# Kernel optimization log

Measured on AMD Instinct MI355X. Metric: run time of the kernel, lower is better.

The kernel has to match this reference:

```python
import jax, jax.numpy as jnp
import numpy as np

B, N, D_IN, D_OUT = 2, 4096, 768, 768


def setup_inputs() -> dict:
    key = jax.random.key(0)
    kx, kq, kk, kv = jax.random.split(key, 4)
    x = jax.random.normal(kx, (B, N, D_IN), dtype=jnp.float32)
    # Linear(d_in, d_out, bias=False) weights, stored as [d_in, d_out]
    scale = 1.0 / np.sqrt(D_IN)
    Wq = jax.random.normal(kq, (D_IN, D_OUT), dtype=jnp.float32) * scale
    Wk = jax.random.normal(kk, (D_IN, D_OUT), dtype=jnp.float32) * scale
    Wv = jax.random.normal(kv, (D_IN, D_OUT), dtype=jnp.float32) * scale
    return {"x": x, "Wq": Wq, "Wk": Wk, "Wv": Wv}


def reference(x, Wq, Wk, Wv):
    # q,k,v: [B, N, D_OUT]
    q = jnp.einsum('bnd,de->bne', x, Wq)
    k = jnp.einsum('bnd,de->bne', x, Wk)
    v = jnp.einsum('bnd,de->bne', x, Wv)
    # Full [B, N, N] score matrix (naive attention, as in source).
    # NOTE: source's masked_fill is non-in-place and discarded, so NO causal
    # mask is actually applied -- reproduced faithfully here.
    scores = jnp.einsum('bqe,bke->bqk', q, k) / jnp.sqrt(jnp.float32(k.shape[-1]))
    weights = jax.nn.softmax(scores, axis=-1)
    # dropout rate 0.0 / eval mode -> identity
    out = jnp.einsum('bqk,bke->bqe', weights, v)  # [B, N, D_OUT]
    return out
```

## Files before the change

kernel.cpp:

```cpp
#include <hip/hip_runtime.h>

typedef __bf16 bf16x8 __attribute__((ext_vector_type(8)));
typedef float f32x4 __attribute__((ext_vector_type(4)));
typedef unsigned short us8 __attribute__((ext_vector_type(8)));

#define GAS __attribute__((address_space(1)))
#define LAS __attribute__((address_space(3)))

__device__ __forceinline__ unsigned short f32_to_bf16(float f) {
    unsigned int u = __float_as_uint(f);
    u += 0x7FFFu + ((u >> 16) & 1u);
    return (unsigned short)(u >> 16);
}

__device__ __forceinline__ float bf16_to_f32(unsigned short h) {
    return __uint_as_float((unsigned int)h << 16);
}

__device__ __forceinline__ void load16(const unsigned short* g, unsigned short* l) {
    __builtin_amdgcn_global_load_lds((GAS unsigned int*)g, (LAS unsigned int*)l, 16, 0, 0);
}

__global__ __launch_bounds__(1024) void prep(
    const float* __restrict__ x, unsigned short* __restrict__ Xbf,
    const float* __restrict__ W0, const float* __restrict__ W1, const float* __restrict__ W2,
    unsigned short* __restrict__ T0, unsigned short* __restrict__ T1, unsigned short* __restrict__ T2)
{
    __shared__ float tile[32][33];
    const int id = blockIdx.x;
    const int t = threadIdx.x;
    if (id < 1536) {
        int i = id * 1024 + t;
        float4 v = ((const float4*)x)[i];
        ushort4 o;
        o.x = f32_to_bf16(v.x); o.y = f32_to_bf16(v.y);
        o.z = f32_to_bf16(v.z); o.w = f32_to_bf16(v.w);
        ((ushort4*)Xbf)[i] = o;
    } else {
        const int tid = id - 1536;
        const int z = tid / 576, rem = tid % 576;
        const int by = rem / 24, bx = rem % 24;
        const float* W = (z == 0) ? W0 : (z == 1) ? W1 : W2;
        unsigned short* T = (z == 0) ? T0 : (z == 1) ? T1 : T2;
        const int r0 = by * 32, c0 = bx * 32;
        const int tx = t & 31, ty = t >> 5;
        tile[ty][tx] = W[(size_t)(r0 + ty) * 768 + c0 + tx];
        __syncthreads();
        T[(size_t)(c0 + ty) * 768 + r0 + tx] = f32_to_bf16(tile[tx][ty]);
    }
}

__device__ __forceinline__ void qk_body(
    unsigned short* smem, int f,
    const unsigned short* __restrict__ Xbf, const unsigned short* __restrict__ Wqk,
    unsigned short* __restrict__ Qb, unsigned short* __restrict__ Kb)
{
    const int xcd = f & 7;
    const int local = f >> 3;
    const int mb = xcd * 4 + (local >> 3);
    const int nb = local & 7;
    unsigned short* AsP[2] = { smem, smem + 16384 };
    unsigned short* BsP[2] = { smem + 32768, smem + 32768 + 12288 };
    const unsigned short* A = Xbf;
    const unsigned short* B = Wqk;
    unsigned short* C = (nb < 4) ? Qb : Kb;
    const int m0 = mb * 256;
    const int n0 = nb * 192;
    const int c0 = (nb & 3) * 192;
    const int lda = 768, ldb = 768, ldc = 768;
    constexpr int NT = 12;

    const int t = threadIdx.x;
    const int lane = t & 63;
    const int w = t >> 6;
    const int wm = (w >> 2) * 128;
    const int wn = (w & 3) * 48;
    const int r15 = lane & 15;
    const int qa = lane >> 4;

    const unsigned short* srcA[4];
    int dstA[4];
#pragma unroll
    for (int i = 0; i < 4; ++i) {
        const int c = i * 512 + t;
        const int row = c >> 3;
        const int cc = (c & 7) ^ (row & 7);
        srcA[i] = A + (size_t)(m0 + row) * lda + cc * 8;
        dstA[i] = c * 8;
    }
    const unsigned short* srcB[3];
    int dstB[3];
#pragma unroll
    for (int i = 0; i < 3; ++i) {
        const int c = i * 512 + t;
        const int row = c >> 3;
        const int cc = (c & 7) ^ (row & 7);
        srcB[i] = B + (size_t)(n0 + row) * ldb + cc * 8;
        dstB[i] = c * 8;
    }

    auto stage = [&](int buf, int kbase) {
#pragma unroll
        for (int i = 0; i < 4; ++i) load16(srcA[i] + kbase, &AsP[buf][dstA[i]]);
#pragma unroll
        for (int i = 0; i < 3; ++i) load16(srcB[i] + kbase, &BsP[buf][dstB[i]]);
    };

    int offA[8][2], offB[3][2];
#pragma unroll
    for (int mi = 0; mi < 8; ++mi) {
        const int row = wm + mi * 16 + r15;
#pragma unroll
        for (int ks = 0; ks < 2; ++ks)
            offA[mi][ks] = row * 64 + (((ks << 2) + qa) ^ (row & 7)) * 8;
    }
#pragma unroll
    for (int ni = 0; ni < 3; ++ni) {
        const int row = wn + ni * 16 + r15;
#pragma unroll
        for (int ks = 0; ks < 2; ++ks)
            offB[ni][ks] = row * 64 + (((ks << 2) + qa) ^ (row & 7)) * 8;
    }

    f32x4 acc[8][3];
#pragma unroll
    for (int i = 0; i < 8; ++i)
#pragma unroll
        for (int j = 0; j < 3; ++j) acc[i][j] = (f32x4){0.f, 0.f, 0.f, 0.f};

    stage(0, 0);
    stage(1, 64);

    for (int tt = 0; tt < NT; ++tt) {
        const int b = tt & 1;
        if (tt == NT - 1) {
            asm volatile("s_waitcnt vmcnt(0)" ::: "memory");
        } else {
            asm volatile("s_waitcnt vmcnt(7)" ::: "memory");
        }
        __builtin_amdgcn_s_barrier();

#pragma unroll
        for (int ks = 0; ks < 2; ++ks) {
            bf16x8 aA[8], bB[3];
#pragma unroll
            for (int i = 0; i < 8; ++i)
                aA[i] = *(const bf16x8*)&AsP[b][offA[i][ks]];
#pragma unroll
            for (int ni = 0; ni < 3; ++ni)
                bB[ni] = *(const bf16x8*)&BsP[b][offB[ni][ks]];
#pragma unroll
            for (int i = 0; i < 8; ++i)
#pragma unroll
                for (int ni = 0; ni < 3; ++ni)
                    acc[i][ni] = __builtin_amdgcn_mfma_f32_16x16x32_bf16(
                        aA[i], bB[ni], acc[i][ni], 0, 0, 0);
        }

        asm volatile("" ::: "memory");
        __builtin_amdgcn_s_barrier();

        if (tt + 2 < NT) stage(b, (tt + 2) << 6);
    }

    const int cr = (lane >> 4) * 4;
#pragma unroll
    for (int mi = 0; mi < 8; ++mi)
#pragma unroll
        for (int ni = 0; ni < 3; ++ni) {
            const int gm = m0 + wm + mi * 16 + cr;
            const int gn = c0 + wn + ni * 16 + r15;
#pragma unroll
            for (int r = 0; r < 4; ++r)
                C[(size_t)(gm + r) * ldc + gn] = f32_to_bf16(acc[mi][ni][r]);
        }
}

__device__ __forceinline__ void vt_body(
    unsigned short* smem, int f,
    const unsigned short* __restrict__ WvT, const unsigned short* __restrict__ Xbf,
    unsigned short* __restrict__ Vt)
{
    const int xcd = f & 7;
    const int local = f >> 3;
    const int nb = xcd * 8 + (local >> 2);
    const int mb = local & 3;
    unsigned short* AsP[2] = { smem, smem + 12288 };
    unsigned short* BsP[2] = { smem + 24576, smem + 24576 + 8192 };
    const unsigned short* A = WvT;
    const unsigned short* B = Xbf;
    unsigned short* C = Vt;
    const int m0 = mb * 192;
    const int n0 = nb * 128;
    const int lda = 768, ldb = 768, ldc = 8192;
    constexpr int NT = 12;

    const int t = threadIdx.x;
    const int lane = t & 63;
    const int w = t >> 6;
    const int wm = (w >> 2) * 96;
    const int wn = (w & 3) * 32;
    const int r15 = lane & 15;
    const int qa = lane >> 4;

    const unsigned short* srcA[3];
    int dstA[3];
#pragma unroll
    for (int i = 0; i < 3; ++i) {
        const int c = i * 512 + t;
        const int row = c >> 3;
        const int cc = (c & 7) ^ (row & 7);
        srcA[i] = A + (size_t)(m0 + row) * lda + cc * 8;
        dstA[i] = c * 8;
    }
    const unsigned short* srcB[2];
    int dstB[2];
#pragma unroll
    for (int i = 0; i < 2; ++i) {
        const int c = i * 512 + t;
        const int row = c >> 3;
        const int cc = (c & 7) ^ (row & 7);
        srcB[i] = B + (size_t)(n0 + row) * ldb + cc * 8;
        dstB[i] = c * 8;
    }

    auto stage = [&](int buf, int kbase) {
#pragma unroll
        for (int i = 0; i < 3; ++i) load16(srcA[i] + kbase, &AsP[buf][dstA[i]]);
#pragma unroll
        for (int i = 0; i < 2; ++i) load16(srcB[i] + kbase, &BsP[buf][dstB[i]]);
    };

    int offA[6][2], offB[2][2];
#pragma unroll
    for (int mi = 0; mi < 6; ++mi) {
        const int row = wm + mi * 16 + r15;
#pragma unroll
        for (int ks = 0; ks < 2; ++ks)
            offA[mi][ks] = row * 64 + (((ks << 2) + qa) ^ (row & 7)) * 8;
    }
#pragma unroll
    for (int ni = 0; ni < 2; ++ni) {
        const int row = wn + ni * 16 + r15;
#pragma unroll
        for (int ks = 0; ks < 2; ++ks)
            offB[ni][ks] = row * 64 + (((ks << 2) + qa) ^ (row & 7)) * 8;
    }

    f32x4 acc[6][2];
#pragma unroll
    for (int i = 0; i < 6; ++i)
#pragma unroll
        for (int j = 0; j < 2; ++j) acc[i][j] = (f32x4){0.f, 0.f, 0.f, 0.f};

    stage(0, 0);
    stage(1, 64);

    for (int tt = 0; tt < NT; ++tt) {
        const int b = tt & 1;
        if (tt == NT - 1) {
            asm volatile("s_waitcnt vmcnt(0)" ::: "memory");
        } else {
            asm volatile("s_waitcnt vmcnt(5)" ::: "memory");
        }
        __builtin_amdgcn_s_barrier();

#pragma unroll
        for (int ks = 0; ks < 2; ++ks) {
            bf16x8 aA[6], bB[2];
#pragma unroll
            for (int i = 0; i < 6; ++i)
                aA[i] = *(const bf16x8*)&AsP[b][offA[i][ks]];
#pragma unroll
            for (int ni = 0; ni < 2; ++ni)
                bB[ni] = *(const bf16x8*)&BsP[b][offB[ni][ks]];
#pragma unroll
            for (int i = 0; i < 6; ++i)
#pragma unroll
                for (int ni = 0; ni < 2; ++ni)
                    acc[i][ni] = __builtin_amdgcn_mfma_f32_16x16x32_bf16(
                        aA[i], bB[ni], acc[i][ni], 0, 0, 0);
        }

        asm volatile("" ::: "memory");
        __builtin_amdgcn_s_barrier();

        if (tt + 2 < NT) stage(b, (tt + 2) << 6);
    }

    const int cr = (lane >> 4) * 4;
#pragma unroll
    for (int mi = 0; mi < 6; ++mi)
#pragma unroll
        for (int ni = 0; ni < 2; ++ni) {
            const int gm = m0 + wm + mi * 16 + cr;
            const int gn = n0 + wn + ni * 16 + r15;
#pragma unroll
            for (int r = 0; r < 4; ++r)
                C[(size_t)(gm + r) * ldc + gn] = f32_to_bf16(acc[mi][ni][r]);
        }
}

__global__ __launch_bounds__(512) void qkv3(
    const unsigned short* __restrict__ Xbf,
    const unsigned short* __restrict__ Wqk,
    unsigned short* __restrict__ Qb,
    unsigned short* __restrict__ Kb,
    unsigned short* __restrict__ Vt)
{
    __shared__ unsigned short smem[57344];
    const int f = blockIdx.x;
    if (f < 256) qk_body(smem, f, Xbf, Wqk, Qb, Kb);
    else         vt_body(smem, f - 256, Wqk + 1179648, Xbf, Vt);
}

__global__ __launch_bounds__(512) void gemm_s_exp2(
    const unsigned short* __restrict__ Q, const unsigned short* __restrict__ Kb,
    unsigned short* __restrict__ Sexp, float alpha)
{
    const int f = blockIdx.x;
    const int xcd = f & 7;
    const int local = f >> 3;
    const int x = (xcd & 1) * 8 + (local & 7);
    const int y = ((xcd >> 1) & 1) * 8 + (local >> 3);
    const int bb = xcd >> 2;
    const unsigned short* A = Q + (size_t)bb * 3145728;
    const unsigned short* B = Kb + (size_t)bb * 3145728;
    unsigned short* C = Sexp + (size_t)bb * 16777216;
    const int m0 = y * 256, n0 = x * 256;
    const int lda = 768, ldb = 768, ldc = 4096;
    constexpr int NT = 12;

    __shared__ unsigned short As[2][256 * 64];
    __shared__ unsigned short Bs[2][256 * 64];

    const int t = threadIdx.x;
    const int lane = t & 63;
    const int w = t >> 6;
    const int wm = (w >> 2) * 128;
    const int wn = (w & 3) * 64;
    const int r15 = lane & 15;
    const int qa = lane >> 4;

    const unsigned short* srcA[4];
    const unsigned short* srcB[4];
    int dst[4];
#pragma unroll
    for (int i = 0; i < 4; ++i) {
        const int c = i * 512 + t;
        const int row = c >> 3;
        const int cc = (c & 7) ^ (row & 7);
        srcA[i] = A + (size_t)(m0 + row) * lda + cc * 8;
        srcB[i] = B + (size_t)(n0 + row) * ldb + cc * 8;
        dst[i] = c * 8;
    }

    auto stage = [&](int buf, int kbase) {
#pragma unroll
        for (int i = 0; i < 4; ++i)
            load16(srcA[i] + kbase, &As[buf][dst[i]]);
#pragma unroll
        for (int i = 0; i < 4; ++i)
            load16(srcB[i] + kbase, &Bs[buf][dst[i]]);
    };

    int offA[8][2], offB[4][2];
#pragma unroll
    for (int mi = 0; mi < 8; ++mi) {
        const int row = wm + mi * 16 + r15;
#pragma unroll
        for (int ks = 0; ks < 2; ++ks)
            offA[mi][ks] = row * 64 + (((ks << 2) + qa) ^ (row & 7)) * 8;
    }
#pragma unroll
    for (int ni = 0; ni < 4; ++ni) {
        const int row = wn + ni * 16 + r15;
#pragma unroll
        for (int ks = 0; ks < 2; ++ks)
            offB[ni][ks] = row * 64 + (((ks << 2) + qa) ^ (row & 7)) * 8;
    }

    f32x4 acc[8][4];
#pragma unroll
    for (int i = 0; i < 8; ++i)
#pragma unroll
        for (int j = 0; j < 4; ++j) acc[i][j] = (f32x4){0.f, 0.f, 0.f, 0.f};

    stage(0, 0);
    stage(1, 64);

    for (int tt = 0; tt < NT; ++tt) {
        const int b = tt & 1;
        if (tt == NT - 1) {
            asm volatile("s_waitcnt vmcnt(0)" ::: "memory");
        } else {
            asm volatile("s_waitcnt vmcnt(8)" ::: "memory");
        }
        __builtin_amdgcn_s_barrier();

#pragma unroll
        for (int ks = 0; ks < 2; ++ks) {
            bf16x8 aA[8], bB[4];
#pragma unroll
            for (int i = 0; i < 8; ++i)
                aA[i] = *(const bf16x8*)&As[b][offA[i][ks]];
#pragma unroll
            for (int ni = 0; ni < 4; ++ni)
                bB[ni] = *(const bf16x8*)&Bs[b][offB[ni][ks]];
#pragma unroll
            for (int i = 0; i < 8; ++i)
#pragma unroll
                for (int ni = 0; ni < 4; ++ni)
                    acc[i][ni] = __builtin_amdgcn_mfma_f32_16x16x32_bf16(
                        aA[i], bB[ni], acc[i][ni], 0, 0, 0);
        }

        asm volatile("" ::: "memory");
        __builtin_amdgcn_s_barrier();

        if (tt + 2 < NT) stage(b, (tt + 2) << 6);
    }

    const int cr = (lane >> 4) * 4;
#pragma unroll
    for (int mi = 0; mi < 8; ++mi)
#pragma unroll
        for (int ni = 0; ni < 4; ++ni) {
            const int gm = m0 + wm + mi * 16 + cr;
            const int gn = n0 + wn + ni * 16 + r15;
#pragma unroll
            for (int r = 0; r < 4; ++r)
                C[(size_t)(gm + r) * ldc + gn] =
                    f32_to_bf16(__expf(alpha * acc[mi][ni][r]));
        }
}

__global__ __launch_bounds__(512) void gemm_out(
    const unsigned short* __restrict__ P, const unsigned short* __restrict__ Vt,
    float* __restrict__ out)
{
    const int f = blockIdx.x;
    const int xcd = f & 7;
    const int local = f >> 3;
    const int nb = local & 3;
    const int rg = xcd * 8 + (local >> 2);
    const int batch = rg >> 5;
    const int mb = rg & 31;
    const unsigned short* A = P + (size_t)batch * 16777216;
    const unsigned short* B = Vt + (size_t)batch * 4096;
    float* C = out + (size_t)batch * 3145728;
    const int m0 = mb * 128, n0 = nb * 192;
    const int lda = 4096, ldb = 8192;
    constexpr int NT = 64;

    __shared__ unsigned short As[3][128 * 64];
    __shared__ unsigned short Bs[3][192 * 64];
    __shared__ float lsum_lds[128];

    const int t = threadIdx.x;
    const int lane = t & 63;
    const int w = t >> 6;
    const int wm = (w >> 2) * 64;
    const int wn = (w & 3) * 48;
    const int r15 = lane & 15;
    const int qa = lane >> 4;

    const unsigned short* srcA[2];
    int dstA[2];
#pragma unroll
    for (int i = 0; i < 2; ++i) {
        const int c = i * 512 + t;
        const int row = c >> 3;
        const int cc = (c & 7) ^ (row & 7);
        srcA[i] = A + (size_t)(m0 + row) * lda + cc * 8;
        dstA[i] = c * 8;
    }
    const unsigned short* srcB[3];
    int dstB[3];
#pragma unroll
    for (int i = 0; i < 3; ++i) {
        const int c = i * 512 + t;
        const int row = c >> 3;
        const int cc = (c & 7) ^ (row & 7);
        srcB[i] = B + (size_t)(n0 + row) * ldb + cc * 8;
        dstB[i] = c * 8;
    }

    auto stage = [&](int buf, int kbase) {
#pragma unroll
        for (int i = 0; i < 2; ++i)
            load16(srcA[i] + kbase, &As[buf][dstA[i]]);
#pragma unroll
        for (int i = 0; i < 3; ++i)
            load16(srcB[i] + kbase, &Bs[buf][dstB[i]]);
    };

    int offA[4][2], offB[3][2];
#pragma unroll
    for (int mi = 0; mi < 4; ++mi) {
        const int row = wm + mi * 16 + r15;
#pragma unroll
        for (int ks = 0; ks < 2; ++ks)
            offA[mi][ks] = row * 64 + (((ks << 2) + qa) ^ (row & 7)) * 8;
    }
#pragma unroll
    for (int ni = 0; ni < 3; ++ni) {
        const int row = wn + ni * 16 + r15;
#pragma unroll
        for (int ks = 0; ks < 2; ++ks)
            offB[ni][ks] = row * 64 + (((ks << 2) + qa) ^ (row & 7)) * 8;
    }

    f32x4 acc[4][3];
#pragma unroll
    for (int i = 0; i < 4; ++i)
#pragma unroll
        for (int j = 0; j < 3; ++j) acc[i][j] = (f32x4){0.f, 0.f, 0.f, 0.f};
    float rsum = 0.f;

    stage(0, 0);
    stage(1, 64);
    stage(2, 128);

    int b = 0;
    for (int tt = 0; tt < NT; ++tt) {
        if (tt < NT - 2) {
            asm volatile("s_waitcnt vmcnt(10)" ::: "memory");
        } else if (tt == NT - 2) {
            asm volatile("s_waitcnt vmcnt(5)" ::: "memory");
        } else {
            asm volatile("s_waitcnt vmcnt(0)" ::: "memory");
        }
        __builtin_amdgcn_s_barrier();

#pragma unroll
        for (int ks = 0; ks < 2; ++ks) {
            bf16x8 aA[4], bB[3];
#pragma unroll
            for (int i = 0; i < 4; ++i)
                aA[i] = *(const bf16x8*)&As[b][offA[i][ks]];
#pragma unroll
            for (int ni = 0; ni < 3; ++ni)
                bB[ni] = *(const bf16x8*)&Bs[b][offB[ni][ks]];
#pragma unroll
            for (int i = 0; i < 4; ++i)
#pragma unroll
                for (int ni = 0; ni < 3; ++ni)
                    acc[i][ni] = __builtin_amdgcn_mfma_f32_16x16x32_bf16(
                        aA[i], bB[ni], acc[i][ni], 0, 0, 0);
        }

        {
            const us8* rp = (const us8*)&As[b][(t >> 2) * 64 + (t & 3) * 16];
            us8 v0 = rp[0], v1 = rp[1];
#pragma unroll
            for (int j = 0; j < 8; ++j)
                rsum += bf16_to_f32(v0[j]) + bf16_to_f32(v1[j]);
        }

        asm volatile("" ::: "memory");
        __builtin_amdgcn_s_barrier();

        if (tt + 3 < NT) stage(b, (tt + 3) << 6);
        b = (b == 2) ? 0 : b + 1;
    }

    rsum += __shfl_xor(rsum, 1, 64);
    rsum += __shfl_xor(rsum, 2, 64);
    if ((t & 3) == 0) lsum_lds[t >> 2] = rsum;
    __syncthreads();

    const int cr = (lane >> 4) * 4;
#pragma unroll
    for (int mi = 0; mi < 4; ++mi) {
        const int lr = wm + mi * 16 + cr;
        const int gm = m0 + lr;
        const float i0 = 1.f / lsum_lds[lr + 0];
        const float i1 = 1.f / lsum_lds[lr + 1];
        const float i2 = 1.f / lsum_lds[lr + 2];
        const float i3 = 1.f / lsum_lds[lr + 3];
#pragma unroll
        for (int ni = 0; ni < 3; ++ni) {
            const int gn = n0 + wn + ni * 16 + r15;
            C[(size_t)(gm + 0) * 768 + gn] = acc[mi][ni][0] * i0;
            C[(size_t)(gm + 1) * 768 + gn] = acc[mi][ni][1] * i1;
            C[(size_t)(gm + 2) * 768 + gn] = acc[mi][ni][2] * i2;
            C[(size_t)(gm + 3) * 768 + gn] = acc[mi][ni][3] * i3;
        }
    }
}

extern "C" void kernel_launch(void* const* d_in, const int* in_sizes, int n_in,
                              void* d_out, int out_size, void* d_ws, size_t ws_size,
                              hipStream_t stream) {
    const float* x  = (const float*)d_in[0];
    const float* Wq = (const float*)d_in[1];
    const float* Wk = (const float*)d_in[2];
    const float* Wv = (const float*)d_in[3];
    float* out = (float*)d_out;

    char* base = (char*)d_ws;
    size_t off = 0;
    auto alloc = [&](size_t b) { char* p = base + off; off += (b + 255) & ~(size_t)255; return p; };

    unsigned short* Xbf = (unsigned short*)alloc(8192ull * 768 * 2);
    unsigned short* WqT = (unsigned short*)alloc(768ull * 768 * 2);
    unsigned short* WkT = (unsigned short*)alloc(768ull * 768 * 2);
    unsigned short* WvT = (unsigned short*)alloc(768ull * 768 * 2);
    unsigned short* Qb  = (unsigned short*)alloc(8192ull * 768 * 2);
    unsigned short* Kb  = (unsigned short*)alloc(8192ull * 768 * 2);
    unsigned short* Vt  = (unsigned short*)alloc(768ull * 8192 * 2);
    unsigned short* Sexp = (unsigned short*)alloc(2ull * 4096 * 4096 * 2);
    (void)ws_size; (void)in_sizes; (void)n_in; (void)out_size; (void)WkT; (void)WvT;

    prep<<<dim3(3264), dim3(1024), 0, stream>>>(x, Xbf, Wq, Wk, Wv, WqT, WkT, WvT);
    qkv3<<<dim3(512), dim3(512), 0, stream>>>(Xbf, WqT, Qb, Kb, Vt);
    gemm_s_exp2<<<dim3(512), dim3(512), 0, stream>>>(
        Qb, Kb, Sexp, 0.03608439182435161f);
    gemm_out<<<dim3(256), dim3(512), 0, stream>>>(Sexp, Vt, out);
}
```

Baseline: 248.4 us.

## Interleave S-GEMM loads with MFMA phases and reshape row-sum LDS reads

The QK^T exp GEMM main loop is split into eight phases per pair of K tiles. Each phase issues a quarter of the next tile's global-to-LDS loads, holds a barrier, raises wave priority around its MFMA block, and waits on vmcnt only at half-tile boundaries, so memory traffic is spread across the compute. In the output GEMM, the per-row exp-sum now reads LDS with one contiguous 16-byte chunk per thread at two strided offsets and reduces over 8 lanes instead of 4. This is meant to avoid LDS bank conflicts in that reduction. The finer-grained barriers add synchronisation overhead, and the hand-set vmcnt accounting has to stay correct.

```diff
diff --git a/kernel.cpp b/kernel.cpp
--- a/kernel.cpp
+++ b/kernel.cpp
@@ -314,7 +314,7 @@
     else         vt_body(smem, f - 256, Wqk + 1179648, Xbf, Vt);
 }
 
-__global__ __launch_bounds__(512) void gemm_s_exp2(
+__global__ __launch_bounds__(512) void gemm_s_exp8(
     const unsigned short* __restrict__ Q, const unsigned short* __restrict__ Kb,
     unsigned short* __restrict__ Sexp, float alpha)
 {
@@ -355,13 +355,13 @@
         dst[i] = c * 8;
     }
 
-    auto stage = [&](int buf, int kbase) {
-#pragma unroll
-        for (int i = 0; i < 4; ++i)
-            load16(srcA[i] + kbase, &As[buf][dst[i]]);
-#pragma unroll
-        for (int i = 0; i < 4; ++i)
-            load16(srcB[i] + kbase, &Bs[buf][dst[i]]);
+    auto stageA = [&](int buf, int kbase, int h) {
+        load16(srcA[2 * h]     + kbase, &As[buf][dst[2 * h]]);
+        load16(srcA[2 * h + 1] + kbase, &As[buf][dst[2 * h + 1]]);
+    };
+    auto stageB = [&](int buf, int kbase, int h) {
+        load16(srcB[2 * h]     + kbase, &Bs[buf][dst[2 * h]]);
+        load16(srcB[2 * h + 1] + kbase, &Bs[buf][dst[2 * h + 1]]);
     };
 
     int offA[8][2], offB[4][2];
@@ -386,40 +386,57 @@
 #pragma unroll
         for (int j = 0; j < 4; ++j) acc[i][j] = (f32x4){0.f, 0.f, 0.f, 0.f};
 
-    stage(0, 0);
-    stage(1, 64);
-
-    for (int tt = 0; tt < NT; ++tt) {
-        const int b = tt & 1;
-        if (tt == NT - 1) {
-            asm volatile("s_waitcnt vmcnt(0)" ::: "memory");
-        } else {
-            asm volatile("s_waitcnt vmcnt(8)" ::: "memory");
-        }
-        __builtin_amdgcn_s_barrier();
-
-#pragma unroll
-        for (int ks = 0; ks < 2; ++ks) {
-            bf16x8 aA[8], bB[4];
-#pragma unroll
-            for (int i = 0; i < 8; ++i)
-                aA[i] = *(const bf16x8*)&As[b][offA[i][ks]];
-#pragma unroll
-            for (int ni = 0; ni < 4; ++ni)
-                bB[ni] = *(const bf16x8*)&Bs[b][offB[ni][ks]];
-#pragma unroll
-            for (int i = 0; i < 8; ++i)
-#pragma unroll
-                for (int ni = 0; ni < 4; ++ni)
-                    acc[i][ni] = __builtin_amdgcn_mfma_f32_16x16x32_bf16(
-                        aA[i], bB[ni], acc[i][ni], 0, 0, 0);
-        }
-
-        asm volatile("" ::: "memory");
-        __builtin_amdgcn_s_barrier();
-
-        if (tt + 2 < NT) stage(b, (tt + 2) << 6);
-    }
+#define PHASE(BUF, KS, AH, STG, VMC)                                          \
+    {                                                                         \
+        bf16x8 aA[4], bB[4];                                                  \
+        _Pragma("unroll")                                                     \
+        for (int i = 0; i < 4; ++i)                                           \
+            aA[i] = *(const bf16x8*)&As[BUF][offA[(AH) * 4 + i][KS]];         \
+        _Pragma("unroll")                                                     \
+        for (int ni = 0; ni < 4; ++ni)                                        \
+            bB[ni] = *(const bf16x8*)&Bs[BUF][offB[ni][KS]];                  \
+        STG;                                                                  \
+        __builtin_amdgcn_s_barrier();                                         \
+        asm volatile("s_waitcnt lgkmcnt(0)" ::: "memory");                    \
+        __builtin_amdgcn_s_setprio(1);                                        \
+        _Pragma("unroll")                                                     \
+        for (int i = 0; i < 4; ++i)                                           \
+            _Pragma("unroll")                                                 \
+            for (int ni = 0; ni < 4; ++ni)                                    \
+                acc[(AH) * 4 + i][ni] = __builtin_amdgcn_mfma_f32_16x16x32_bf16( \
+                    aA[i], bB[ni], acc[(AH) * 4 + i][ni], 0, 0, 0);           \
+        __builtin_amdgcn_s_setprio(0);                                        \
+        {                                                                     \
+            int _vm = (VMC);                                                  \
+            if (_vm == 2)      asm volatile("s_waitcnt vmcnt(2)" ::: "memory"); \
+            else if (_vm == 0) asm volatile("s_waitcnt vmcnt(0)" ::: "memory"); \
+        }                                                                     \
+        __builtin_amdgcn_s_barrier();                                         \
+    }
+
+    stageA(0, 0, 0); stageA(0, 0, 1); stageB(0, 0, 0); stageB(0, 0, 1);
+    stageA(1, 64, 0); stageA(1, 64, 1); stageB(1, 64, 0); stageB(1, 64, 1);
+    asm volatile("s_waitcnt vmcnt(8)" ::: "memory");
+    __builtin_amdgcn_s_barrier();
+
+    for (int u = 0; u < NT / 2; ++u) {
+        const bool s01 = (u > 0);
+        const bool s2  = (2 * u + 2 < NT);
+        const bool s3  = (2 * u + 3 < NT);
+        const int k1 = (2 * u + 1) << 6;
+        const int k2 = (2 * u + 2) << 6;
+        const int k3 = (2 * u + 3) << 6;
+
+        PHASE(0, 0, 0, { if (s01) stageA(1, k1, 1); }, -1)
+        PHASE(0, 1, 0, { if (s01) stageB(1, k1, 0); }, -1)
+        PHASE(0, 0, 1, { if (s01) stageB(1, k1, 1); }, -1)
+        PHASE(0, 1, 1, { if (s2)  stageA(0, k2, 0); }, (s2 ? 2 : 0))
+        PHASE(1, 0, 0, { if (s2)  stageA(0, k2, 1); }, -1)
+        PHASE(1, 1, 0, { if (s2)  stageB(0, k2, 0); }, -1)
+        PHASE(1, 0, 1, { if (s2)  stageB(0, k2, 1); }, -1)
+        PHASE(1, 1, 1, { if (s3)  stageA(1, k3, 0); }, (s3 ? 2 : 0))
+    }
+#undef PHASE
 
     const int cr = (lane >> 4) * 4;
 #pragma unroll
@@ -516,7 +533,7 @@
     for (int i = 0; i < 4; ++i)
 #pragma unroll
         for (int j = 0; j < 3; ++j) acc[i][j] = (f32x4){0.f, 0.f, 0.f, 0.f};
-    float rsum = 0.f;
+    float rsumA = 0.f, rsumB = 0.f;
 
     stage(0, 0);
     stage(1, 64);
@@ -551,11 +568,14 @@
         }
 
         {
-            const us8* rp = (const us8*)&As[b][(t >> 2) * 64 + (t & 3) * 16];
-            us8 v0 = rp[0], v1 = rp[1];
-#pragma unroll
-            for (int j = 0; j < 8; ++j)
-                rsum += bf16_to_f32(v0[j]) + bf16_to_f32(v1[j]);
+            const us8* fp = (const us8*)As[b];
+            us8 v0 = fp[t];
+            us8 v1 = fp[t + 512];
+#pragma unroll
+            for (int j = 0; j < 8; ++j) {
+                rsumA += bf16_to_f32(v0[j]);
+                rsumB += bf16_to_f32(v1[j]);
+            }
         }
 
         asm volatile("" ::: "memory");
@@ -565,9 +585,16 @@
         b = (b == 2) ? 0 : b + 1;
     }
 
-    rsum += __shfl_xor(rsum, 1, 64);
-    rsum += __shfl_xor(rsum, 2, 64);
-    if ((t & 3) == 0) lsum_lds[t >> 2] = rsum;
+    rsumA += __shfl_xor(rsumA, 1, 64);
+    rsumA += __shfl_xor(rsumA, 2, 64);
+    rsumA += __shfl_xor(rsumA, 4, 64);
+    rsumB += __shfl_xor(rsumB, 1, 64);
+    rsumB += __shfl_xor(rsumB, 2, 64);
+    rsumB += __shfl_xor(rsumB, 4, 64);
+    if ((t & 7) == 0) {
+        lsum_lds[t >> 3] = rsumA;
+        lsum_lds[64 + (t >> 3)] = rsumB;
+    }
     __syncthreads();
 
     const int cr = (lane >> 4) * 4;
@@ -615,7 +642,7 @@
 
     prep<<<dim3(3264), dim3(1024), 0, stream>>>(x, Xbf, Wq, Wk, Wv, WqT, WkT, WvT);
     qkv3<<<dim3(512), dim3(512), 0, stream>>>(Xbf, WqT, Qb, Kb, Vt);
-    gemm_s_exp2<<<dim3(512), dim3(512), 0, stream>>>(
+    gemm_s_exp8<<<dim3(512), dim3(512), 0, stream>>>(
         Qb, Kb, Sexp, 0.03608439182435161f);
     gemm_out<<<dim3(256), dim3(512), 0, stream>>>(Sexp, Vt, out);
 }
```

Measured after the change: 254.3 us. 2.4% more time.
